# Optimization experiments

Hardware: AMD Instinct MI355X
Metric: run time of the kernel (lower is better)

Reference implementation:

```python
import jax, jax.numpy as jnp
import numpy as np

H = W = 128          # image_size
K = 8                # faces_per_pixel
EPS = 1e-8
BIG = 1e10           # sentinel z for non-covering faces


def _rasterize(vertices, faces):
    # vertices: (B, V, 3) NDC x,y (+x left, +y up, pytorch3d convention), camera z > 0
    # faces:    (B, F, 3) int indices into V
    fv = jax.vmap(lambda v, f: v[f])(vertices, faces)  # (B, F, 3, 3)
    vx, vy, vz = fv[..., 0], fv[..., 1], fv[..., 2]     # (B, F, 3)

    def e(a):
        return a[:, None, None, :]                      # (B, 1, 1, F)

    x0, x1, x2 = e(vx[..., 0]), e(vx[..., 1]), e(vx[..., 2])
    y0, y1, y2 = e(vy[..., 0]), e(vy[..., 1]), e(vy[..., 2])
    z0, z1, z2 = e(vz[..., 0]), e(vz[..., 1]), e(vz[..., 2])

    dt = vertices.dtype
    PX = (1.0 - 2.0 * (jnp.arange(W, dtype=dt) + 0.5) / W)[None, None, :, None]  # (1,1,W,1)
    PY = (1.0 - 2.0 * (jnp.arange(H, dtype=dt) + 0.5) / H)[None, :, None, None]  # (1,H,1,1)

    def edge_fn(ax, ay, bx, by):
        # signed area of (a, b, pixel); broadcasts to (B, H, W, F)
        return (bx - ax) * (PY - ay) - (by - ay) * (PX - ax)

    w0 = edge_fn(x1, y1, x2, y2)
    w1 = edge_fn(x2, y2, x0, y0)
    w2 = edge_fn(x0, y0, x1, y1)
    area = (x1 - x0) * (y2 - y0) - (y1 - y0) * (x2 - x0)       # (B,1,1,F)
    area_safe = jnp.where(jnp.abs(area) < EPS, EPS, area)

    # screen-space barycentrics
    b0 = w0 / area_safe
    b1 = w1 / area_safe
    b2 = w2 / area_safe
    inside = (b0 >= 0) & (b1 >= 0) & (b2 >= 0) & (jnp.abs(area) > EPS)

    # perspective-correct barycentrics (pytorch3d barycentric_perspective_correct)
    n0 = b0 * z1 * z2
    n1 = z0 * b1 * z2
    n2 = z0 * z1 * b2
    den = n0 + n1 + n2
    den_safe = jnp.where(jnp.abs(den) < EPS, EPS, den)
    p0 = n0 / den_safe
    p1 = n1 / den_safe
    p2 = n2 / den_safe

    zpix = p0 * z0 + p1 * z1 + p2 * z2                          # (B,H,W,F)
    zs = jnp.where(inside, zpix, BIG)

    # per-pixel nearest-K z-buffer over all faces
    negz, idx = jax.lax.top_k(-zs, K)                           # (B,H,W,K)
    zbuf = -negz
    valid = zbuf < 0.5 * BIG
    pix_to_face = jnp.where(valid, idx, -1)

    g = lambda a: jnp.take_along_axis(a, idx, axis=-1)
    bary = jnp.stack([g(p0), g(p1), g(p2)], axis=-1)            # (B,H,W,K,3)
    bary = jnp.where(valid[..., None], bary, -1.0)
    zbuf = jnp.where(valid, zbuf, -1.0)

    # signed squared NDC distance of pixel to nearest triangle edge (negative inside)
    def edge_d2(ax, ay, bx, by):
        ex = bx - ax
        ey = by - ay
        l2 = jnp.maximum(ex * ex + ey * ey, EPS)
        t = jnp.clip(((PX - ax) * ex + (PY - ay) * ey) / l2, 0.0, 1.0)
        dx = PX - (ax + t * ex)
        dy = PY - (ay + t * ey)
        return dx * dx + dy * dy

    d2 = jnp.minimum(edge_d2(x0, y0, x1, y1),
                     jnp.minimum(edge_d2(x1, y1, x2, y2), edge_d2(x2, y2, x0, y0)))
    sd = jnp.where(inside, -d2, d2)
    dists = jnp.where(valid, g(sd), -1.0)                       # (B,H,W,K)

    return pix_to_face, zbuf, bary, dists


def setup_inputs() -> dict:
    key = jax.random.key(0)
    k1, k2, k3 = jax.random.split(key, 3)
    B, V, F = 1, 600, 1000
    xy = jax.random.uniform(k1, (B, V, 2), minval=-1.0, maxval=1.0)
    z = jax.random.uniform(k2, (B, V, 1), minval=1.0, maxval=3.0)
    vertices = jnp.concatenate([xy, z], axis=-1)
    faces = jax.random.randint(k3, (B, F, 3), 0, V)
    return {"vertices": vertices, "faces": faces}


def reference(vertices, faces):
    # Fragments: (pix_to_face, zbuf, bary_coords, dists)
    return _rasterize(vertices, faces)
```

## Files before the change

kernel.cpp:

```cpp
#include <hip/hip_runtime.h>


#define HW_    128
#define KF     8
#define NPIX   (HW_ * HW_)
#define EPSf   1e-8f
#define BIGf   1e10f
#define NPB    16
#define CH     32
#define SCAP   512
#define BBMARG 1e-4f
#define EDGEM  1e-3f

typedef unsigned long long ull;

#define CE(X, Y) { ull _mn = (X) < (Y) ? (X) : (Y); ull _mx = (X) < (Y) ? (Y) : (X); (X) = _mn; (Y) = _mx; }

__device__ __forceinline__ void merge_lists(ull* cand, int la, int lb, int p) {
    ull a[8], b[8], c[8];
#pragma unroll
    for (int i = 0; i < 8; ++i) a[i] = cand[i * 512 + la * 16 + p];
#pragma unroll
    for (int i = 0; i < 8; ++i) b[i] = cand[i * 512 + lb * 16 + p];
#pragma unroll
    for (int i = 0; i < 8; ++i) { ull x = a[i], y = b[7 - i]; c[i] = x < y ? x : y; }
    CE(c[0], c[4]); CE(c[1], c[5]); CE(c[2], c[6]); CE(c[3], c[7]);
    CE(c[0], c[2]); CE(c[1], c[3]); CE(c[4], c[6]); CE(c[5], c[7]);
    CE(c[0], c[1]); CE(c[2], c[3]); CE(c[4], c[5]); CE(c[6], c[7]);
#pragma unroll
    for (int i = 0; i < 8; ++i) cand[i * 512 + la * 16 + p] = c[i];
}

__device__ __forceinline__ float edge_d2_fn(float px, float py,
                                            float ax, float ay,
                                            float bx, float by) {
#pragma clang fp contract(off)
    float ex = bx - ax;
    float ey = by - ay;
    float l2 = fmaxf(ex * ex + ey * ey, EPSf);
    float t  = ((px - ax) * ex + (py - ay) * ey) / l2;
    t = fminf(fmaxf(t, 0.0f), 1.0f);
    float dx = px - (ax + t * ex);
    float dy = py - (ay + t * ey);
    return dx * dx + dy * dy;
}

__global__ __launch_bounds__(256) void preprocess_kernel(
    const float* __restrict__ verts,
    const int* __restrict__ faces,
    float4* __restrict__ ws4,
    int F)
{
#pragma clang fp contract(off)
    int f = blockIdx.x * 256 + threadIdx.x;
    if (f >= F) return;
    int i0 = faces[3 * f + 0];
    int i1 = faces[3 * f + 1];
    int i2 = faces[3 * f + 2];
    float x0 = verts[3 * i0 + 0], y0 = verts[3 * i0 + 1], z0 = verts[3 * i0 + 2];
    float x1 = verts[3 * i1 + 0], y1 = verts[3 * i1 + 1], z1 = verts[3 * i1 + 2];
    float x2 = verts[3 * i2 + 0], y2 = verts[3 * i2 + 1], z2 = verts[3 * i2 + 2];
    float area = (x1 - x0) * (y2 - y0) - (y1 - y0) * (x2 - x0);
    float s = (area > 0.0f) ? 1.0f : -1.0f;
    float B0 = (x2 - x1), C0 = -(y2 - y1), A0 = (y2 - y1) * x1 - (x2 - x1) * y1;
    float B1 = (x0 - x2), C1 = -(y0 - y2), A1 = (y0 - y2) * x2 - (x0 - x2) * y2;
    float B2 = (x1 - x0), C2 = -(y1 - y0), A2 = (y1 - y0) * x0 - (x1 - x0) * y0;
    float4* p = ws4 + f * 7;
    p[0] = make_float4(fminf(x0, fminf(x1, x2)) - BBMARG,
                       fmaxf(x0, fmaxf(x1, x2)) + BBMARG,
                       fminf(y0, fminf(y1, y2)) - BBMARG,
                       fmaxf(y0, fmaxf(y1, y2)) + BBMARG);
    p[1] = make_float4(s * A0, s * B0, s * C0, 0.0f);
    p[2] = make_float4(s * A1, s * B1, s * C1, 0.0f);
    p[3] = make_float4(s * A2, s * B2, s * C2, 0.0f);
    p[4] = make_float4(x0, y0, x1, y1);
    p[5] = make_float4(x2, y2, z0, z1);
    p[6] = make_float4(z2, area, (float)f, 0.0f);
}

__global__ __launch_bounds__(512, 8) void raster_kernel(
    const float4* __restrict__ ws4,
    float* __restrict__ out,
    int F)
{
#pragma clang fp contract(off)
    __shared__ __align__(16) char smem[32832];
    float4*   ga   = (float4*)smem;
    float4*   gb   = (float4*)(smem + 8192);
    float4*   gzf  = (float4*)(smem + 16384);
    unsigned* wtot = (unsigned*)(smem + 32768);
    ull*      cand = (ull*)smem;

    int tid  = threadIdx.x;
    int tile = blockIdx.x;
    int txi = tile & 31, tyi = tile >> 5;

    float pxhi = 1.0f - (2.0f * ((float)(txi * 4)     + 0.5f)) / 128.0f;
    float pxlo = 1.0f - (2.0f * ((float)(txi * 4 + 3) + 0.5f)) / 128.0f;
    float pyhi = 1.0f - (2.0f * ((float)(tyi * 4)     + 0.5f)) / 128.0f;
    float pylo = 1.0f - (2.0f * ((float)(tyi * 4 + 3) + 0.5f)) / 128.0f;

    int lane = tid & 63;
    int wv   = tid >> 6;
    int S = 0;

    for (int fbase = 0; fbase < F; fbase += 512) {
        int f = fbase + tid;
        bool keep = false;
        const float4* p = ws4 + f * 7;
        if (f < F) {
            float4 b4 = p[0];
            float4 e0 = p[1];
            float4 e1 = p[2];
            float4 e2 = p[3];
            bool bo = (b4.x <= pxhi) && (b4.y >= pxlo) && (b4.z <= pyhi) && (b4.w >= pylo);
            float w0m = e0.x + fmaxf(e0.y * pylo, e0.y * pyhi) + fmaxf(e0.z * pxlo, e0.z * pxhi);
            float w1m = e1.x + fmaxf(e1.y * pylo, e1.y * pyhi) + fmaxf(e1.z * pxlo, e1.z * pxhi);
            float w2m = e2.x + fmaxf(e2.y * pylo, e2.y * pyhi) + fmaxf(e2.z * pxlo, e2.z * pxhi);
            keep = bo && (w0m >= -EDGEM) && (w1m >= -EDGEM) && (w2m >= -EDGEM);
        }
        ull bal = __ballot(keep);
        int below = __popcll(bal & ((1ull << lane) - 1ull));
        if (lane == 0) wtot[wv] = (unsigned)__popcll(bal);
        __syncthreads();
        int pre = 0, tot = 0;
#pragma unroll
        for (int w8 = 0; w8 < 8; ++w8) {
            int t = (int)wtot[w8];
            if (w8 < wv) pre += t;
            tot += t;
        }
        if (keep) {
            int pos = S + pre + below;
            if (pos < SCAP) {
                ga[pos]  = p[4];
                gb[pos]  = p[5];
                gzf[pos] = p[6];
            }
        }
        S += tot;
        if (S > SCAP) S = SCAP;
        __syncthreads();
    }

    int p_ = tid & 15;
    int c = tid >> 4;
    int w = txi * 4 + (p_ & 3);
    int h = tyi * 4 + (p_ >> 2);
    float px = 1.0f - (2.0f * ((float)w + 0.5f)) / 128.0f;
    float py = 1.0f - (2.0f * ((float)h + 0.5f)) / 128.0f;

    float tz[KF];
    int   ti_[KF];
#pragma unroll
    for (int k = 0; k < KF; ++k) { tz[k] = BIGf; ti_[k] = -1; }

    int j0 = (S * c) / CH;
    int j1 = (S * (c + 1)) / CH;
    for (int j = j0; j < j1; ++j) {
        float4 A  = ga[j];
        float4 Bv = gb[j];
        float4 Zf = gzf[j];
        float x0 = A.x,  y0 = A.y,  x1 = A.z,  y1 = A.w;
        float x2 = Bv.x, y2 = Bv.y, z0 = Bv.z, z1 = Bv.w;
        float z2 = Zf.x, area = Zf.y;

        float w0 = (x2 - x1) * (py - y1) - (y2 - y1) * (px - x1);
        float w1 = (x0 - x2) * (py - y2) - (y0 - y2) * (px - x2);
        float w2 = (x1 - x0) * (py - y0) - (y1 - y0) * (px - x0);
        float aabs = fabsf(area);
        float s = (area > 0.0f) ? 1.0f : -1.0f;
        if (!(w0 * s >= 0.0f && w1 * s >= 0.0f && w2 * s >= 0.0f && aabs > EPSf))
            continue;

        float b0 = w0 / area;
        float b1 = w1 / area;
        float b2 = w2 / area;
        float n0 = b0 * z1 * z2;
        float n1 = z0 * b1 * z2;
        float n2 = z0 * z1 * b2;
        float den = n0 + n1 + n2;
        float dabs = fabsf(den);
        float den_safe = (dabs < EPSf) ? EPSf : den;
        float p0 = n0 / den_safe;
        float p1 = n1 / den_safe;
        float p2 = n2 / den_safe;
        float z = p0 * z0 + p1 * z1 + p2 * z2;

        if (z < tz[KF - 1]) {
            int fidx = (int)Zf.z;
            tz[KF - 1] = z;
            ti_[KF - 1] = fidx;
#pragma unroll
            for (int k = KF - 1; k > 0; --k) {
                bool sw = tz[k] < tz[k - 1];
                float az = sw ? tz[k - 1] : tz[k];
                float bz = sw ? tz[k]     : tz[k - 1];
                int   ai = sw ? ti_[k - 1] : ti_[k];
                int   bi = sw ? ti_[k]     : ti_[k - 1];
                tz[k] = az; tz[k - 1] = bz;
                ti_[k] = ai; ti_[k - 1] = bi;
            }
        }
    }

    __syncthreads();
#pragma unroll
    for (int k = 0; k < KF; ++k)
        cand[k * 512 + c * 16 + p_] =
            ((ull)__float_as_uint(tz[k]) << 32) | (ull)(unsigned)ti_[k];
    __syncthreads();

    if (tid < 256) { int pp = tid & 15, r = tid >> 4; merge_lists(cand,  2 * r,  2 * r + 1, pp); }
    __syncthreads();
    if (tid < 128) { int pp = tid & 15, r = tid >> 4; merge_lists(cand,  4 * r,  4 * r + 2, pp); }
    __syncthreads();
    if (tid < 64)  { int pp = tid & 15, r = tid >> 4; merge_lists(cand,  8 * r,  8 * r + 4, pp); }
    __syncthreads();
    if (tid < 32)  { int pp = tid & 15, r = tid >> 4; merge_lists(cand, 16 * r, 16 * r + 8, pp); }
    __syncthreads();
    if (tid < 16)  { merge_lists(cand, 0, 16, tid); }
    __syncthreads();

    if (tid < NPB * KF) {
        int pp = tid >> 3;
        int k  = tid & 7;
        ull key = cand[k * 512 + pp];
        unsigned idxu = (unsigned)(key & 0xFFFFFFFFULL);
        float zk = __uint_as_float((unsigned)(key >> 32));

        int w2i = txi * 4 + (pp & 3);
        int h2i = tyi * 4 + (pp >> 2);
        float qx = 1.0f - (2.0f * ((float)w2i + 0.5f)) / 128.0f;
        float qy = 1.0f - (2.0f * ((float)h2i + 0.5f)) / 128.0f;
        int base = (h2i * HW_ + w2i) * KF;

        float vp = -1.0f, vz = -1.0f, vb0 = -1.0f, vb1 = -1.0f, vb2 = -1.0f, vd = -1.0f;
        if (idxu != 0xFFFFFFFFu) {
            int f = (int)idxu;
            const float4* pw = ws4 + f * 7;
            float4 A4 = pw[4];
            float4 B4 = pw[5];
            float4 Z4 = pw[6];
            float x0 = A4.x, y0 = A4.y, x1 = A4.z, y1 = A4.w;
            float x2 = B4.x, y2 = B4.y, z0 = B4.z, z1 = B4.w;
            float z2 = Z4.x, area = Z4.y;
            float w0 = (x2 - x1) * (qy - y1) - (y2 - y1) * (qx - x1);
            float w1 = (x0 - x2) * (qy - y2) - (y0 - y2) * (qx - x2);
            float w2 = (x1 - x0) * (qy - y0) - (y1 - y0) * (qx - x0);
            float aabs = fabsf(area);
            float area_safe = (aabs < EPSf) ? EPSf : area;
            float b0 = w0 / area_safe;
            float b1 = w1 / area_safe;
            float b2 = w2 / area_safe;
            float n0 = b0 * z1 * z2;
            float n1 = z0 * b1 * z2;
            float n2 = z0 * z1 * b2;
            float den = n0 + n1 + n2;
            float dabs = fabsf(den);
            float den_safe = (dabs < EPSf) ? EPSf : den;
            float p0 = n0 / den_safe;
            float p1 = n1 / den_safe;
            float p2 = n2 / den_safe;
            float e0 = edge_d2_fn(qx, qy, x0, y0, x1, y1);
            float e1 = edge_d2_fn(qx, qy, x1, y1, x2, y2);
            float e2 = edge_d2_fn(qx, qy, x2, y2, x0, y0);
            float d2 = fminf(e0, fminf(e1, e2));
            vp = (float)f;
            vz = zk;
            vb0 = p0; vb1 = p1; vb2 = p2;
            vd = -d2;
        }

        float* o_pix = out;
        float* o_z   = out + NPIX * KF;
        float* o_b   = out + 2 * NPIX * KF;
        float* o_d   = out + 2 * NPIX * KF + NPIX * KF * 3;
        o_pix[base + k] = vp;
        o_z[base + k]   = vz;
        o_b[(base + k) * 3 + 0] = vb0;
        o_b[(base + k) * 3 + 1] = vb1;
        o_b[(base + k) * 3 + 2] = vb2;
        o_d[base + k]   = vd;
    }
}

extern "C" void kernel_launch(void* const* d_in, const int* in_sizes, int n_in,
                              void* d_out, int out_size, void* d_ws, size_t ws_size,
                              hipStream_t stream) {
    const float* verts = (const float*)d_in[0];
    const int* faces = (const int*)d_in[1];
    float* out = (float*)d_out;
    float4* ws4 = (float4*)d_ws;
    int F = in_sizes[1] / 3;
    preprocess_kernel<<<dim3((F + 255) / 256), dim3(256), 0, stream>>>(verts, faces, ws4, F);
    raster_kernel<<<dim3(1024), dim3(512), 0, stream>>>(ws4, out, F);
}
```

Measured before the change: 88.95 us.

## Replace shared-memory merge tree with wavefront shuffle top-K merge

Each pixel's 32 face-chunk workers now sit in one half of a wavefront, and their per-thread top-8 lists are merged with xor-shuffle bitonic steps instead of a five-level shared-memory merge tree with block barriers. The candidate lists are kept as packed 64-bit z/index keys, and the output stage reads the merged key straight from registers. This removes the shared candidate buffer, several __syncthreads, and LDS traffic, and shrinks shared memory. The cost is more 64-bit shuffle and compare instructions per thread, and the partial top-K insertion now works on 64-bit keys.

Result: faster. 86.84 us (-2.4%).

```diff
diff --git a/kernel.cpp b/kernel.cpp
--- a/kernel.cpp
+++ b/kernel.cpp
@@ -6,8 +6,6 @@
 #define NPIX   (HW_ * HW_)
 #define EPSf   1e-8f
 #define BIGf   1e10f
-#define NPB    16
-#define CH     32
 #define SCAP   512
 #define BBMARG 1e-4f
 #define EDGEM  1e-3f
@@ -15,21 +13,6 @@
 typedef unsigned long long ull;
 
 #define CE(X, Y) { ull _mn = (X) < (Y) ? (X) : (Y); ull _mx = (X) < (Y) ? (Y) : (X); (X) = _mn; (Y) = _mx; }
-
-__device__ __forceinline__ void merge_lists(ull* cand, int la, int lb, int p) {
-    ull a[8], b[8], c[8];
-#pragma unroll
-    for (int i = 0; i < 8; ++i) a[i] = cand[i * 512 + la * 16 + p];
-#pragma unroll
-    for (int i = 0; i < 8; ++i) b[i] = cand[i * 512 + lb * 16 + p];
-#pragma unroll
-    for (int i = 0; i < 8; ++i) { ull x = a[i], y = b[7 - i]; c[i] = x < y ? x : y; }
-    CE(c[0], c[4]); CE(c[1], c[5]); CE(c[2], c[6]); CE(c[3], c[7]);
-    CE(c[0], c[2]); CE(c[1], c[3]); CE(c[4], c[6]); CE(c[5], c[7]);
-    CE(c[0], c[1]); CE(c[2], c[3]); CE(c[4], c[5]); CE(c[6], c[7]);
-#pragma unroll
-    for (int i = 0; i < 8; ++i) cand[i * 512 + la * 16 + p] = c[i];
-}
 
 __device__ __forceinline__ float edge_d2_fn(float px, float py,
                                             float ax, float ay,
@@ -84,12 +67,11 @@
     int F)
 {
 #pragma clang fp contract(off)
-    __shared__ __align__(16) char smem[32832];
+    __shared__ __align__(16) char smem[24608];
     float4*   ga   = (float4*)smem;
     float4*   gb   = (float4*)(smem + 8192);
     float4*   gzf  = (float4*)(smem + 16384);
-    unsigned* wtot = (unsigned*)(smem + 32768);
-    ull*      cand = (ull*)smem;
+    unsigned* wtot = (unsigned*)(smem + 24576);
 
     int tid  = threadIdx.x;
     int tile = blockIdx.x;
@@ -143,20 +125,20 @@
         __syncthreads();
     }
 
-    int p_ = tid & 15;
-    int c = tid >> 4;
+    int p_ = (wv << 1) | (lane >> 5);
+    int c  = lane & 31;
     int w = txi * 4 + (p_ & 3);
     int h = tyi * 4 + (p_ >> 2);
     float px = 1.0f - (2.0f * ((float)w + 0.5f)) / 128.0f;
     float py = 1.0f - (2.0f * ((float)h + 0.5f)) / 128.0f;
 
-    float tz[KF];
-    int   ti_[KF];
-#pragma unroll
-    for (int k = 0; k < KF; ++k) { tz[k] = BIGf; ti_[k] = -1; }
-
-    int j0 = (S * c) / CH;
-    int j1 = (S * (c + 1)) / CH;
+    const ull SENT = ((ull)0x501502F9u << 32) | 0xFFFFFFFFull;
+    ull tk[KF];
+#pragma unroll
+    for (int k = 0; k < KF; ++k) tk[k] = SENT;
+
+    int j0 = (S * c) >> 5;
+    int j1 = (S * (c + 1)) >> 5;
     for (int j = j0; j < j1; ++j) {
         float4 A  = ga[j];
         float4 Bv = gb[j];
@@ -187,56 +169,42 @@
         float p2 = n2 / den_safe;
         float z = p0 * z0 + p1 * z1 + p2 * z2;
 
-        if (z < tz[KF - 1]) {
-            int fidx = (int)Zf.z;
-            tz[KF - 1] = z;
-            ti_[KF - 1] = fidx;
-#pragma unroll
-            for (int k = KF - 1; k > 0; --k) {
-                bool sw = tz[k] < tz[k - 1];
-                float az = sw ? tz[k - 1] : tz[k];
-                float bz = sw ? tz[k]     : tz[k - 1];
-                int   ai = sw ? ti_[k - 1] : ti_[k];
-                int   bi = sw ? ti_[k]     : ti_[k - 1];
-                tz[k] = az; tz[k - 1] = bz;
-                ti_[k] = ai; ti_[k - 1] = bi;
-            }
-        }
-    }
-
-    __syncthreads();
-#pragma unroll
-    for (int k = 0; k < KF; ++k)
-        cand[k * 512 + c * 16 + p_] =
-            ((ull)__float_as_uint(tz[k]) << 32) | (ull)(unsigned)ti_[k];
-    __syncthreads();
-
-    if (tid < 256) { int pp = tid & 15, r = tid >> 4; merge_lists(cand,  2 * r,  2 * r + 1, pp); }
-    __syncthreads();
-    if (tid < 128) { int pp = tid & 15, r = tid >> 4; merge_lists(cand,  4 * r,  4 * r + 2, pp); }
-    __syncthreads();
-    if (tid < 64)  { int pp = tid & 15, r = tid >> 4; merge_lists(cand,  8 * r,  8 * r + 4, pp); }
-    __syncthreads();
-    if (tid < 32)  { int pp = tid & 15, r = tid >> 4; merge_lists(cand, 16 * r, 16 * r + 8, pp); }
-    __syncthreads();
-    if (tid < 16)  { merge_lists(cand, 0, 16, tid); }
-    __syncthreads();
-
-    if (tid < NPB * KF) {
-        int pp = tid >> 3;
-        int k  = tid & 7;
-        ull key = cand[k * 512 + pp];
+        ull key = ((ull)__float_as_uint(z) << 32) | (ull)(unsigned)(int)Zf.z;
+        if (key < tk[KF - 1]) {
+            tk[KF - 1] = key;
+#pragma unroll
+            for (int k = KF - 1; k > 0; --k) CE(tk[k - 1], tk[k]);
+        }
+    }
+
+#pragma unroll
+    for (int d = 1; d < 32; d <<= 1) {
+        ull cc[KF];
+#pragma unroll
+        for (int i = 0; i < KF; ++i) {
+            ull bv = (ull)__shfl_xor((long long)tk[KF - 1 - i], d, 64);
+            cc[i] = tk[i] < bv ? tk[i] : bv;
+        }
+        CE(cc[0], cc[4]); CE(cc[1], cc[5]); CE(cc[2], cc[6]); CE(cc[3], cc[7]);
+        CE(cc[0], cc[2]); CE(cc[1], cc[3]); CE(cc[4], cc[6]); CE(cc[5], cc[7]);
+        CE(cc[0], cc[1]); CE(cc[2], cc[3]); CE(cc[4], cc[5]); CE(cc[6], cc[7]);
+#pragma unroll
+        for (int i = 0; i < KF; ++i) tk[i] = cc[i];
+    }
+
+    int sub = lane & 31;
+    ull key = tk[0];
+#pragma unroll
+    for (int k = 1; k < KF; ++k) key = (sub == k) ? tk[k] : key;
+
+    if (sub < KF) {
+        int k = sub;
         unsigned idxu = (unsigned)(key & 0xFFFFFFFFULL);
         float zk = __uint_as_float((unsigned)(key >> 32));
-
-        int w2i = txi * 4 + (pp & 3);
-        int h2i = tyi * 4 + (pp >> 2);
-        float qx = 1.0f - (2.0f * ((float)w2i + 0.5f)) / 128.0f;
-        float qy = 1.0f - (2.0f * ((float)h2i + 0.5f)) / 128.0f;
-        int base = (h2i * HW_ + w2i) * KF;
+        int base = (h * HW_ + w) * KF;
 
         float vp = -1.0f, vz = -1.0f, vb0 = -1.0f, vb1 = -1.0f, vb2 = -1.0f, vd = -1.0f;
-        if (idxu != 0xFFFFFFFFu) {
+        if (idxu != 0xFFFFFFFFu && zk < 0.5f * BIGf) {
             int f = (int)idxu;
             const float4* pw = ws4 + f * 7;
             float4 A4 = pw[4];
@@ -245,9 +213,9 @@
             float x0 = A4.x, y0 = A4.y, x1 = A4.z, y1 = A4.w;
             float x2 = B4.x, y2 = B4.y, z0 = B4.z, z1 = B4.w;
             float z2 = Z4.x, area = Z4.y;
-            float w0 = (x2 - x1) * (qy - y1) - (y2 - y1) * (qx - x1);
-            float w1 = (x0 - x2) * (qy - y2) - (y0 - y2) * (qx - x2);
-            float w2 = (x1 - x0) * (qy - y0) - (y1 - y0) * (qx - x0);
+            float w0 = (x2 - x1) * (py - y1) - (y2 - y1) * (px - x1);
+            float w1 = (x0 - x2) * (py - y2) - (y0 - y2) * (px - x2);
+            float w2 = (x1 - x0) * (py - y0) - (y1 - y0) * (px - x0);
             float aabs = fabsf(area);
             float area_safe = (aabs < EPSf) ? EPSf : area;
             float b0 = w0 / area_safe;
@@ -262,9 +230,9 @@
             float p0 = n0 / den_safe;
             float p1 = n1 / den_safe;
             float p2 = n2 / den_safe;
-            float e0 = edge_d2_fn(qx, qy, x0, y0, x1, y1);
-            float e1 = edge_d2_fn(qx, qy, x1, y1, x2, y2);
-            float e2 = edge_d2_fn(qx, qy, x2, y2, x0, y0);
+            float e0 = edge_d2_fn(px, py, x0, y0, x1, y1);
+            float e1 = edge_d2_fn(px, py, x1, y1, x2, y2);
+            float e2 = edge_d2_fn(px, py, x2, y2, x0, y0);
             float d2 = fminf(e0, fminf(e1, e2));
             vp = (float)f;
             vz = zk;
```
